# Kernel tuning notes

Hardware: AMD Instinct MI355X
Metric: run time of the kernel (lower is better)

## Reference

```python
import jax, jax.numpy as jnp
import numpy as np

EPS = 1e-06

def _feature_map(x):
    # elu(x) + 1, positive feature map
    return jax.nn.elu(x) + 1.0

def setup_inputs() -> dict:
    key = jax.random.key(0)
    k1, k2, k3 = jax.random.split(key, 3)
    B, L, d_k, d_v = 2, 4096, 128, 128
    Q = jax.random.normal(k1, (B, L, d_k), dtype=jnp.float32)
    K = jax.random.normal(k2, (B, L, d_k), dtype=jnp.float32)
    V = jax.random.normal(k3, (B, L, d_v), dtype=jnp.float32)
    return {"Q": Q, "K": K, "V": V}

def reference(Q, K, V):
    # Causal linear attention (ELU feature map).
    # out_l = phi(Q_l) @ sum_{j<=l} phi(K_j)^T V_j
    # Z_l   = phi(Q_l) . sum_{j<=l} phi(K_j)
    phiQ = _feature_map(Q)                       # (B, L, dk)
    phiK = _feature_map(K)                       # (B, L, dk)
    # cumulative KV state: (B, L, dk, dv) -- parallel replacement of the
    # original per-step bmm loop
    KV = jnp.cumsum(phiK[..., :, None] * V[..., None, :], axis=1)
    out = jnp.einsum('blk,blkv->blv', phiQ, KV)  # (B, L, dv)
    Kc = jnp.cumsum(phiK, axis=1)                # (B, L, dk)
    Z = jnp.einsum('blk,blk->bl', phiQ, Kc)[..., None]  # (B, L, 1)
    return out / (Z + EPS)
```

## Files before the change

### kernel.cpp

```cpp
#include <hip/hip_runtime.h>


#define EPS 1e-6f

constexpr int Bc = 2;
constexpr int L  = 4096;
constexpr int D  = 128;
constexpr int C  = 128;
constexpr int NC = L / C;
constexpr int P  = 136;

typedef short sh8 __attribute__((ext_vector_type(8)));
typedef float f4  __attribute__((ext_vector_type(4)));

__device__ __forceinline__ float phi(float x) {
    return x > 0.0f ? x + 1.0f : __expf(x);
}
__device__ __forceinline__ unsigned short f2bf(float f) {
    unsigned u = __float_as_uint(f);
    return (unsigned short)((u + 0x7FFFu + ((u >> 16) & 1u)) >> 16);
}
__device__ __forceinline__ float bf2f(unsigned short h) {
    return __uint_as_float(((unsigned)h) << 16);
}
__device__ __forceinline__ sh8 splat1() {
    sh8 s;
#pragma unroll
    for (int j = 0; j < 8; ++j) s[j] = (short)0x3F80;
    return s;
}

__global__ __launch_bounds__(512) void k_prep(
    const float* __restrict__ Q, const float* __restrict__ K,
    const float* __restrict__ V,
    unsigned short* __restrict__ QB, unsigned short* __restrict__ KB,
    unsigned short* __restrict__ KT, unsigned short* __restrict__ VT) {
    const int c = blockIdx.x, b = blockIdx.y, zz = blockIdx.z;
    const int tid = threadIdx.x;
    __shared__ __align__(16) unsigned short sT[128 * P];
    const size_t base  = ((size_t)b * L + (size_t)c * C) * D;
    const size_t tbase = ((size_t)(b * NC + c)) * D * D;

    if (zz == 0) {
        for (int k = 0; k < 8; ++k) {
            int fi = tid + 512 * k;
            int l = fi >> 5, i4 = fi & 31;
            float4 d = *(const float4*)(K + base + (size_t)l * D + i4 * 4);
            unsigned short e0 = f2bf(phi(d.x)), e1 = f2bf(phi(d.y));
            unsigned short e2 = f2bf(phi(d.z)), e3 = f2bf(phi(d.w));
            uint2 pk;
            pk.x = (unsigned)e0 | ((unsigned)e1 << 16);
            pk.y = (unsigned)e2 | ((unsigned)e3 << 16);
            *(uint2*)(KB + base + (size_t)l * D + i4 * 4) = pk;
            int blk = (((l >> 3) + i4) & 15) * 8 + (l & 7);
            sT[(i4 * 4 + 0) * P + blk] = e0;
            sT[(i4 * 4 + 1) * P + blk] = e1;
            sT[(i4 * 4 + 2) * P + blk] = e2;
            sT[(i4 * 4 + 3) * P + blk] = e3;
        }
        __syncthreads();
        for (int k = 0; k < 4; ++k) {
            int fi = tid + 512 * k;
            int i = fi >> 4, lch = fi & 15;
            uint4 dd = *(const uint4*)(sT + i * P + (((lch + (i >> 2)) & 15) * 8));
            *(uint4*)(KT + tbase + (size_t)i * D + lch * 8) = dd;
        }
    } else {
        for (int k = 0; k < 8; ++k) {
            int fi = tid + 512 * k;
            int l = fi >> 5, i4 = fi & 31;
            float4 d = *(const float4*)(V + base + (size_t)l * D + i4 * 4);
            int blk = (((l >> 3) + i4) & 15) * 8 + (l & 7);
            sT[(i4 * 4 + 0) * P + blk] = f2bf(d.x);
            sT[(i4 * 4 + 1) * P + blk] = f2bf(d.y);
            sT[(i4 * 4 + 2) * P + blk] = f2bf(d.z);
            sT[(i4 * 4 + 3) * P + blk] = f2bf(d.w);
        }
        for (int k = 0; k < 8; ++k) {
            int fi = tid + 512 * k;
            int l = fi >> 5, i4 = fi & 31;
            float4 d = *(const float4*)(Q + base + (size_t)l * D + i4 * 4);
            uint2 pk;
            pk.x = (unsigned)f2bf(phi(d.x)) | ((unsigned)f2bf(phi(d.y)) << 16);
            pk.y = (unsigned)f2bf(phi(d.z)) | ((unsigned)f2bf(phi(d.w)) << 16);
            *(uint2*)(QB + base + (size_t)l * D + i4 * 4) = pk;
        }
        __syncthreads();
        for (int k = 0; k < 4; ++k) {
            int fi = tid + 512 * k;
            int v = fi >> 4, lch = fi & 15;
            uint4 dd = *(const uint4*)(sT + v * P + (((lch + (v >> 2)) & 15) * 8));
            *(uint4*)(VT + tbase + (size_t)v * D + lch * 8) = dd;
        }
    }
}

__global__ __launch_bounds__(512) void k1(
    const unsigned short* __restrict__ KT, const unsigned short* __restrict__ VT,
    unsigned short* __restrict__ SB, float* __restrict__ Ksum) {
    const int c = blockIdx.x, b = blockIdx.y, vs = blockIdx.z;
    const int tid = threadIdx.x;
    __shared__ __align__(16) unsigned short sA[64 * P];
    __shared__ __align__(16) unsigned short sKb[128 * P];
    const size_t tbase = ((size_t)(b * NC + c)) * D * D;

    const uint4* vtg = (const uint4*)(VT + tbase + (size_t)vs * 64 * D);
    for (int k = 0; k < 2; ++k) {
        int fi = tid + 512 * k;
        int v = fi >> 4, ch = fi & 15;
        *(uint4*)(sA + v * P + ch * 8) = vtg[fi];
    }
    const uint4* ktg = (const uint4*)(KT + tbase);
    for (int k = 0; k < 4; ++k) {
        int fi = tid + 512 * k;
        int i = fi >> 4, ch = fi & 15;
        *(uint4*)(sKb + i * P + ch * 8) = ktg[fi];
    }
    __syncthreads();

    const int w = tid >> 6, lane = tid & 63;
    const int r = lane & 15, q = lane >> 4;
    const int rbase = (w & 3) * 16;
    const int cbase = (w >> 2) * 64;
    const bool doZ = (vs == 0) && ((w & 3) == 0);
    const sh8 az = splat1();

    f4 acc[4], kz[4];
#pragma unroll
    for (int f = 0; f < 4; ++f) { acc[f] = {0.f,0.f,0.f,0.f}; kz[f] = {0.f,0.f,0.f,0.f}; }
#pragma unroll
    for (int ks = 0; ks < 4; ++ks) {
        sh8 a = *(const sh8*)(sA + (rbase + r) * P + ks * 32 + q * 8);
#pragma unroll
        for (int f = 0; f < 4; ++f) {
            sh8 bb = *(const sh8*)(sKb + (cbase + f * 16 + r) * P + ks * 32 + q * 8);
            acc[f] = __builtin_amdgcn_mfma_f32_16x16x32_bf16(a, bb, acc[f], 0, 0, 0);
            if (doZ) kz[f] = __builtin_amdgcn_mfma_f32_16x16x32_bf16(az, bb, kz[f], 0, 0, 0);
        }
    }
    unsigned short* out = SB + tbase;
#pragma unroll
    for (int f = 0; f < 4; ++f) {
        int i = cbase + f * 16 + r;
#pragma unroll
        for (int e = 0; e < 4; ++e) {
            int v = vs * 64 + rbase + q * 4 + e;
            out[(size_t)v * D + i] = f2bf(acc[f][e]);
        }
    }
    if (doZ && q == 0) {
#pragma unroll
        for (int f = 0; f < 4; ++f)
            Ksum[((size_t)(b * NC + c)) * D + cbase + f * 16 + r] = kz[f][0];
    }
}

__global__ __launch_bounds__(256) void k_scan(unsigned short* __restrict__ SB,
                                              float* __restrict__ Ksum) {
    const int SD = D * D;
    int idx = blockIdx.x * 256 + threadIdx.x;
    if (idx < Bc * SD) {
        int b = idx / SD, e = idx % SD;
        size_t off0 = (size_t)b * NC * SD + e;
        unsigned short vals[NC];
#pragma unroll
        for (int c = 0; c < NC; ++c) vals[c] = SB[off0 + (size_t)c * SD];
        float run = 0.0f;
#pragma unroll
        for (int c = 0; c < NC; ++c) {
            SB[off0 + (size_t)c * SD] = f2bf(run);
            run += bf2f(vals[c]);
        }
    } else if (idx < Bc * SD + Bc * D) {
        int rr = idx - Bc * SD;
        int b = rr >> 7, i = rr & 127;
        size_t off0 = (size_t)b * NC * D + i;
        float vals[NC];
#pragma unroll
        for (int c = 0; c < NC; ++c) vals[c] = Ksum[off0 + (size_t)c * D];
        float run = 0.0f;
#pragma unroll
        for (int c = 0; c < NC; ++c) {
            Ksum[off0 + (size_t)c * D] = run;
            run += vals[c];
        }
    }
}

__global__ __launch_bounds__(512) void k_out(
    const unsigned short* __restrict__ QB, const unsigned short* __restrict__ KB,
    const unsigned short* __restrict__ VT, const unsigned short* __restrict__ SB,
    const float* __restrict__ Ksum, float* __restrict__ Out) {
    const int c = blockIdx.x, b = blockIdx.y, rs = blockIdx.z;
    const int tid = threadIdx.x;
    __shared__ __align__(16) unsigned short sQ[32 * P];
    __shared__ __align__(16) unsigned short sKb[128 * P];
    __shared__ __align__(16) unsigned short sV[128 * P];
    __shared__ __align__(16) unsigned short sAm[32 * P];
    __shared__ float sZ[32];
    const size_t base  = ((size_t)b * L + (size_t)c * C) * D;
    const size_t tbase = ((size_t)(b * NC + c)) * D * D;
    const size_t kb    = ((size_t)(b * NC + c)) * D;

    {
        const uint4* qg = (const uint4*)(QB + base + (size_t)rs * 32 * D);
        int fi = tid;
        *(uint4*)(sQ + (fi >> 4) * P + (fi & 15) * 8) = qg[fi];
        const uint4* kg = (const uint4*)(KB + base);
        for (int k = 0; k < 4; ++k) {
            int f2 = tid + 512 * k;
            *(uint4*)(sKb + (f2 >> 4) * P + (f2 & 15) * 8) = kg[f2];
        }
        const uint4* vg = (const uint4*)(VT + tbase);
        for (int k = 0; k < 4; ++k) {
            int f2 = tid + 512 * k;
            *(uint4*)(sV + (f2 >> 4) * P + (f2 & 15) * 8) = vg[f2];
        }
    }
    __syncthreads();

    const int w = tid >> 6, lane = tid & 63;
    const int r = lane & 15, q = lane >> 4;
    const int rbase = (w & 1) * 16;
    const int cq = w >> 1, cbase = cq * 32;
    const bool doZ = (cq == 3);

    sh8 bzk[4];
    if (doZ) {
#pragma unroll
        for (int ks = 0; ks < 4; ++ks) {
            float4 f0 = *(const float4*)(Ksum + kb + ks * 32 + q * 8);
            float4 f1 = *(const float4*)(Ksum + kb + ks * 32 + q * 8 + 4);
            sh8 t;
            t[0] = (short)f2bf(f0.x); t[1] = (short)f2bf(f0.y);
            t[2] = (short)f2bf(f0.z); t[3] = (short)f2bf(f0.w);
            t[4] = (short)f2bf(f1.x); t[5] = (short)f2bf(f1.y);
            t[6] = (short)f2bf(f1.z); t[7] = (short)f2bf(f1.w);
            bzk[ks] = t;
        }
    }

    f4 a2[2];
#pragma unroll
    for (int f = 0; f < 2; ++f) a2[f] = {0.f,0.f,0.f,0.f};
#pragma unroll
    for (int ks = 0; ks < 4; ++ks) {
        sh8 a = *(const sh8*)(sQ + (rbase + r) * P + ks * 32 + q * 8);
#pragma unroll
        for (int f = 0; f < 2; ++f) {
            sh8 bb = *(const sh8*)(sKb + (cbase + f * 16 + r) * P + ks * 32 + q * 8);
            a2[f] = __builtin_amdgcn_mfma_f32_16x16x32_bf16(a, bb, a2[f], 0, 0, 0);
        }
    }
#pragma unroll
    for (int f = 0; f < 2; ++f) {
        int j = cbase + f * 16 + r;
#pragma unroll
        for (int e = 0; e < 4; ++e) {
            int lr = rbase + q * 4 + e;
            sAm[lr * P + j] = f2bf((j <= rs * 32 + lr) ? a2[f][e] : 0.0f);
        }
    }
    __syncthreads();

    {
        const uint4* sg = (const uint4*)(SB + tbase);
        for (int k = 0; k < 4; ++k) {
            int f2 = tid + 512 * k;
            *(uint4*)(sKb + (f2 >> 4) * P + (f2 & 15) * 8) = sg[f2];
        }
    }

    f4 acc[2], zacc = {0.f,0.f,0.f,0.f};
#pragma unroll
    for (int f = 0; f < 2; ++f) acc[f] = {0.f,0.f,0.f,0.f};
    const sh8 bones = splat1();
#pragma unroll
    for (int ks = 0; ks < 4; ++ks) {
        sh8 a = *(const sh8*)(sAm + (rbase + r) * P + ks * 32 + q * 8);
#pragma unroll
        for (int f = 0; f < 2; ++f) {
            sh8 bb = *(const sh8*)(sV + (cbase + f * 16 + r) * P + ks * 32 + q * 8);
            acc[f] = __builtin_amdgcn_mfma_f32_16x16x32_bf16(a, bb, acc[f], 0, 0, 0);
        }
        if (doZ) zacc = __builtin_amdgcn_mfma_f32_16x16x32_bf16(a, bones, zacc, 0, 0, 0);
    }
    __syncthreads();

#pragma unroll
    for (int ks = 0; ks < 4; ++ks) {
        sh8 a = *(const sh8*)(sQ + (rbase + r) * P + ks * 32 + q * 8);
#pragma unroll
        for (int f = 0; f < 2; ++f) {
            sh8 bb = *(const sh8*)(sKb + (cbase + f * 16 + r) * P + ks * 32 + q * 8);
            acc[f] = __builtin_amdgcn_mfma_f32_16x16x32_bf16(a, bb, acc[f], 0, 0, 0);
        }
        if (doZ) zacc = __builtin_amdgcn_mfma_f32_16x16x32_bf16(a, bzk[ks], zacc, 0, 0, 0);
    }
    if (doZ && r == 0) {
#pragma unroll
        for (int e = 0; e < 4; ++e) sZ[rbase + q * 4 + e] = zacc[e] + EPS;
    }
    __syncthreads();

#pragma unroll
    for (int f = 0; f < 2; ++f) {
        int v = cbase + f * 16 + r;
#pragma unroll
        for (int e = 0; e < 4; ++e) {
            int lr = rbase + q * 4 + e;
            Out[base + (size_t)(rs * 32 + lr) * D + v] = acc[f][e] / sZ[lr];
        }
    }
}

extern "C" void kernel_launch(void* const* d_in, const int* in_sizes, int n_in,
                              void* d_out, int out_size, void* d_ws, size_t ws_size,
                              hipStream_t stream) {
    const float* Q = (const float*)d_in[0];
    const float* K = (const float*)d_in[1];
    const float* V = (const float*)d_in[2];
    float* Out = (float*)d_out;
    constexpr size_t NE = (size_t)Bc * L * D;
    char* w = (char*)d_ws;
    unsigned short* SBw  = (unsigned short*)(w);
    float*          Ksum = (float*)(w + NE * 2);
    unsigned short* QB   = (unsigned short*)(w + NE * 2 + (size_t)Bc * NC * D * 4);
    unsigned short* KB   = QB + NE;
    unsigned short* KT   = KB + NE;
    unsigned short* VT   = KT + NE;

    k_prep<<<dim3(NC, Bc, 2), 512, 0, stream>>>(Q, K, V, QB, KB, KT, VT);
    k1<<<dim3(NC, Bc, 2), 512, 0, stream>>>(KT, VT, SBw, Ksum);
    int total = Bc * D * D + Bc * D;
    k_scan<<<dim3((total + 255) / 256), 256, 0, stream>>>(SBw, Ksum);
    k_out<<<dim3(NC, Bc, 4), 512, 0, stream>>>(QB, KB, VT, SBw, Ksum, Out);
}
```

Baseline: 82.20 us.

## Fuse bf16 conversion and feature map into consumer kernels, drop prep kernel

Removes the separate preprocessing kernel that wrote bf16 copies and transposes of phi(Q), phi(K) and V to workspace. The chunk-state kernel and the output kernel now read fp32 inputs directly, apply the feature map, convert to bf16, and transpose into swizzled shared memory themselves, with MFMA operand reads adjusted to the swizzle. This saves one launch and the intermediate global write/read traffic. In exchange, K and V are read and converted redundantly across the z-split blocks (up to four times for K and V in the output kernel) and fp32 loads double the bytes per element.

Result: faster. 77.74 us (-5.4%).

```diff
diff --git a/kernel.cpp b/kernel.cpp
--- a/kernel.cpp
+++ b/kernel.cpp
@@ -23,6 +23,9 @@
 __device__ __forceinline__ float bf2f(unsigned short h) {
     return __uint_as_float(((unsigned)h) << 16);
 }
+__device__ __forceinline__ unsigned packbf(float a, float b) {
+    return (unsigned)f2bf(a) | ((unsigned)f2bf(b) << 16);
+}
 __device__ __forceinline__ sh8 splat1() {
     sh8 s;
 #pragma unroll
@@ -30,91 +33,34 @@
     return s;
 }
 
-__global__ __launch_bounds__(512) void k_prep(
-    const float* __restrict__ Q, const float* __restrict__ K,
-    const float* __restrict__ V,
-    unsigned short* __restrict__ QB, unsigned short* __restrict__ KB,
-    unsigned short* __restrict__ KT, unsigned short* __restrict__ VT) {
-    const int c = blockIdx.x, b = blockIdx.y, zz = blockIdx.z;
-    const int tid = threadIdx.x;
-    __shared__ __align__(16) unsigned short sT[128 * P];
-    const size_t base  = ((size_t)b * L + (size_t)c * C) * D;
-    const size_t tbase = ((size_t)(b * NC + c)) * D * D;
-
-    if (zz == 0) {
-        for (int k = 0; k < 8; ++k) {
-            int fi = tid + 512 * k;
-            int l = fi >> 5, i4 = fi & 31;
-            float4 d = *(const float4*)(K + base + (size_t)l * D + i4 * 4);
-            unsigned short e0 = f2bf(phi(d.x)), e1 = f2bf(phi(d.y));
-            unsigned short e2 = f2bf(phi(d.z)), e3 = f2bf(phi(d.w));
-            uint2 pk;
-            pk.x = (unsigned)e0 | ((unsigned)e1 << 16);
-            pk.y = (unsigned)e2 | ((unsigned)e3 << 16);
-            *(uint2*)(KB + base + (size_t)l * D + i4 * 4) = pk;
-            int blk = (((l >> 3) + i4) & 15) * 8 + (l & 7);
-            sT[(i4 * 4 + 0) * P + blk] = e0;
-            sT[(i4 * 4 + 1) * P + blk] = e1;
-            sT[(i4 * 4 + 2) * P + blk] = e2;
-            sT[(i4 * 4 + 3) * P + blk] = e3;
-        }
-        __syncthreads();
-        for (int k = 0; k < 4; ++k) {
-            int fi = tid + 512 * k;
-            int i = fi >> 4, lch = fi & 15;
-            uint4 dd = *(const uint4*)(sT + i * P + (((lch + (i >> 2)) & 15) * 8));
-            *(uint4*)(KT + tbase + (size_t)i * D + lch * 8) = dd;
-        }
-    } else {
-        for (int k = 0; k < 8; ++k) {
-            int fi = tid + 512 * k;
-            int l = fi >> 5, i4 = fi & 31;
-            float4 d = *(const float4*)(V + base + (size_t)l * D + i4 * 4);
-            int blk = (((l >> 3) + i4) & 15) * 8 + (l & 7);
-            sT[(i4 * 4 + 0) * P + blk] = f2bf(d.x);
-            sT[(i4 * 4 + 1) * P + blk] = f2bf(d.y);
-            sT[(i4 * 4 + 2) * P + blk] = f2bf(d.z);
-            sT[(i4 * 4 + 3) * P + blk] = f2bf(d.w);
-        }
-        for (int k = 0; k < 8; ++k) {
-            int fi = tid + 512 * k;
-            int l = fi >> 5, i4 = fi & 31;
-            float4 d = *(const float4*)(Q + base + (size_t)l * D + i4 * 4);
-            uint2 pk;
-            pk.x = (unsigned)f2bf(phi(d.x)) | ((unsigned)f2bf(phi(d.y)) << 16);
-            pk.y = (unsigned)f2bf(phi(d.z)) | ((unsigned)f2bf(phi(d.w)) << 16);
-            *(uint2*)(QB + base + (size_t)l * D + i4 * 4) = pk;
-        }
-        __syncthreads();
-        for (int k = 0; k < 4; ++k) {
-            int fi = tid + 512 * k;
-            int v = fi >> 4, lch = fi & 15;
-            uint4 dd = *(const uint4*)(sT + v * P + (((lch + (v >> 2)) & 15) * 8));
-            *(uint4*)(VT + tbase + (size_t)v * D + lch * 8) = dd;
-        }
-    }
-}
-
 __global__ __launch_bounds__(512) void k1(
-    const unsigned short* __restrict__ KT, const unsigned short* __restrict__ VT,
+    const float* __restrict__ K, const float* __restrict__ V,
     unsigned short* __restrict__ SB, float* __restrict__ Ksum) {
     const int c = blockIdx.x, b = blockIdx.y, vs = blockIdx.z;
     const int tid = threadIdx.x;
-    __shared__ __align__(16) unsigned short sA[64 * P];
-    __shared__ __align__(16) unsigned short sKb[128 * P];
-    const size_t tbase = ((size_t)(b * NC + c)) * D * D;
-
-    const uint4* vtg = (const uint4*)(VT + tbase + (size_t)vs * 64 * D);
-    for (int k = 0; k < 2; ++k) {
-        int fi = tid + 512 * k;
-        int v = fi >> 4, ch = fi & 15;
-        *(uint4*)(sA + v * P + ch * 8) = vtg[fi];
-    }
-    const uint4* ktg = (const uint4*)(KT + tbase);
+    __shared__ __align__(16) unsigned short sVT[64 * P];
+    __shared__ __align__(16) unsigned short sKT[128 * P];
+    const size_t base = ((size_t)b * L + (size_t)c * C) * D;
+
     for (int k = 0; k < 4; ++k) {
         int fi = tid + 512 * k;
-        int i = fi >> 4, ch = fi & 15;
-        *(uint4*)(sKb + i * P + ch * 8) = ktg[fi];
+        int l = fi >> 4, c4 = fi & 15;
+        float4 vd = *(const float4*)(V + base + (size_t)l * D + vs * 64 + c4 * 4);
+        int blk = (((l >> 3) + c4) & 15) * 8 + (l & 7);
+        sVT[(c4 * 4 + 0) * P + blk] = f2bf(vd.x);
+        sVT[(c4 * 4 + 1) * P + blk] = f2bf(vd.y);
+        sVT[(c4 * 4 + 2) * P + blk] = f2bf(vd.z);
+        sVT[(c4 * 4 + 3) * P + blk] = f2bf(vd.w);
+    }
+    for (int k = 0; k < 8; ++k) {
+        int fi = tid + 512 * k;
+        int l = fi >> 5, i4 = fi & 31;
+        float4 kd = *(const float4*)(K + base + (size_t)l * D + i4 * 4);
+        int blk = (((l >> 3) + i4) & 15) * 8 + (l & 7);
+        sKT[(i4 * 4 + 0) * P + blk] = f2bf(phi(kd.x));
+        sKT[(i4 * 4 + 1) * P + blk] = f2bf(phi(kd.y));
+        sKT[(i4 * 4 + 2) * P + blk] = f2bf(phi(kd.z));
+        sKT[(i4 * 4 + 3) * P + blk] = f2bf(phi(kd.w));
     }
     __syncthreads();
 
@@ -122,23 +68,26 @@
     const int r = lane & 15, q = lane >> 4;
     const int rbase = (w & 3) * 16;
     const int cbase = (w >> 2) * 64;
-    const bool doZ = (vs == 0) && ((w & 3) == 0);
-    const sh8 az = splat1();
+    const bool doK = ((w & 3) == 0);
+    const sh8 ones = splat1();
 
     f4 acc[4], kz[4];
 #pragma unroll
     for (int f = 0; f < 4; ++f) { acc[f] = {0.f,0.f,0.f,0.f}; kz[f] = {0.f,0.f,0.f,0.f}; }
 #pragma unroll
     for (int ks = 0; ks < 4; ++ks) {
-        sh8 a = *(const sh8*)(sA + (rbase + r) * P + ks * 32 + q * 8);
+        int kq = ks * 4 + q;
+        int vr = rbase + r;
+        sh8 a = *(const sh8*)(sVT + vr * P + ((kq + (vr >> 2)) & 15) * 8);
 #pragma unroll
         for (int f = 0; f < 4; ++f) {
-            sh8 bb = *(const sh8*)(sKb + (cbase + f * 16 + r) * P + ks * 32 + q * 8);
-            acc[f] = __builtin_amdgcn_mfma_f32_16x16x32_bf16(a, bb, acc[f], 0, 0, 0);
-            if (doZ) kz[f] = __builtin_amdgcn_mfma_f32_16x16x32_bf16(az, bb, kz[f], 0, 0, 0);
-        }
-    }
-    unsigned short* out = SB + tbase;
+            int ir = cbase + f * 16 + r;
+            sh8 bk = *(const sh8*)(sKT + ir * P + ((kq + (ir >> 2)) & 15) * 8);
+            acc[f] = __builtin_amdgcn_mfma_f32_16x16x32_bf16(a, bk, acc[f], 0, 0, 0);
+            if (doK) kz[f] = __builtin_amdgcn_mfma_f32_16x16x32_bf16(ones, bk, kz[f], 0, 0, 0);
+        }
+    }
+    unsigned short* out = SB + ((size_t)(b * NC + c)) * D * D;
 #pragma unroll
     for (int f = 0; f < 4; ++f) {
         int i = cbase + f * 16 + r;
@@ -148,7 +97,7 @@
             out[(size_t)v * D + i] = f2bf(acc[f][e]);
         }
     }
-    if (doZ && q == 0) {
+    if (doK && q == 0 && vs == 0) {
 #pragma unroll
         for (int f = 0; f < 4; ++f)
             Ksum[((size_t)(b * NC + c)) * D + cbase + f * 16 + r] = kz[f][0];
@@ -188,34 +137,43 @@
 }
 
 __global__ __launch_bounds__(512) void k_out(
-    const unsigned short* __restrict__ QB, const unsigned short* __restrict__ KB,
-    const unsigned short* __restrict__ VT, const unsigned short* __restrict__ SB,
+    const float* __restrict__ Q, const float* __restrict__ K,
+    const float* __restrict__ V, const unsigned short* __restrict__ SB,
     const float* __restrict__ Ksum, float* __restrict__ Out) {
     const int c = blockIdx.x, b = blockIdx.y, rs = blockIdx.z;
     const int tid = threadIdx.x;
     __shared__ __align__(16) unsigned short sQ[32 * P];
-    __shared__ __align__(16) unsigned short sKb[128 * P];
-    __shared__ __align__(16) unsigned short sV[128 * P];
+    __shared__ __align__(16) unsigned short sK[128 * P];
+    __shared__ __align__(16) unsigned short sVT[128 * P];
     __shared__ __align__(16) unsigned short sAm[32 * P];
     __shared__ float sZ[32];
     const size_t base  = ((size_t)b * L + (size_t)c * C) * D;
-    const size_t tbase = ((size_t)(b * NC + c)) * D * D;
+    const size_t tbase = ((size_t)(b * NC + c)) * (size_t)D * D;
     const size_t kb    = ((size_t)(b * NC + c)) * D;
 
-    {
-        const uint4* qg = (const uint4*)(QB + base + (size_t)rs * 32 * D);
-        int fi = tid;
-        *(uint4*)(sQ + (fi >> 4) * P + (fi & 15) * 8) = qg[fi];
-        const uint4* kg = (const uint4*)(KB + base);
-        for (int k = 0; k < 4; ++k) {
-            int f2 = tid + 512 * k;
-            *(uint4*)(sKb + (f2 >> 4) * P + (f2 & 15) * 8) = kg[f2];
-        }
-        const uint4* vg = (const uint4*)(VT + tbase);
-        for (int k = 0; k < 4; ++k) {
-            int f2 = tid + 512 * k;
-            *(uint4*)(sV + (f2 >> 4) * P + (f2 & 15) * 8) = vg[f2];
-        }
+    for (int k = 0; k < 2; ++k) {
+        int fi = tid + 512 * k;
+        int row = fi >> 5, c4 = fi & 31;
+        float4 qd = *(const float4*)(Q + base + (size_t)(rs * 32 + row) * D + c4 * 4);
+        uint2 pq; pq.x = packbf(phi(qd.x), phi(qd.y)); pq.y = packbf(phi(qd.z), phi(qd.w));
+        *(uint2*)(sQ + row * P + c4 * 4) = pq;
+    }
+    for (int k = 0; k < 8; ++k) {
+        int fi = tid + 512 * k;
+        int row = fi >> 5, c4 = fi & 31;
+        float4 kd = *(const float4*)(K + base + (size_t)row * D + c4 * 4);
+        uint2 pk; pk.x = packbf(phi(kd.x), phi(kd.y)); pk.y = packbf(phi(kd.z), phi(kd.w));
+        *(uint2*)(sK + row * P + c4 * 4) = pk;
+    }
+    for (int k = 0; k < 8; ++k) {
+        int fi = tid + 512 * k;
+        int l = fi >> 5, i4 = fi & 31;
+        float4 vd = *(const float4*)(V + base + (size_t)l * D + i4 * 4);
+        int blk = (((l >> 3) + i4) & 15) * 8 + (l & 7);
+        sVT[(i4 * 4 + 0) * P + blk] = f2bf(vd.x);
+        sVT[(i4 * 4 + 1) * P + blk] = f2bf(vd.y);
+        sVT[(i4 * 4 + 2) * P + blk] = f2bf(vd.z);
+        sVT[(i4 * 4 + 3) * P + blk] = f2bf(vd.w);
     }
     __syncthreads();
 
@@ -248,7 +206,7 @@
         sh8 a = *(const sh8*)(sQ + (rbase + r) * P + ks * 32 + q * 8);
 #pragma unroll
         for (int f = 0; f < 2; ++f) {
-            sh8 bb = *(const sh8*)(sKb + (cbase + f * 16 + r) * P + ks * 32 + q * 8);
+            sh8 bb = *(const sh8*)(sK + (cbase + f * 16 + r) * P + ks * 32 + q * 8);
             a2[f] = __builtin_amdgcn_mfma_f32_16x16x32_bf16(a, bb, a2[f], 0, 0, 0);
         }
     }
@@ -258,7 +216,7 @@
 #pragma unroll
         for (int e = 0; e < 4; ++e) {
             int lr = rbase + q * 4 + e;
-            sAm[lr * P + j] = f2bf((j <= rs * 32 + lr) ? a2[f][e] : 0.0f);
+            sAm[lr * P + j] = f2bf((j <= rs * 32 + lr) ? a2[f][e] : 0.f);
         }
     }
     __syncthreads();
@@ -267,23 +225,25 @@
         const uint4* sg = (const uint4*)(SB + tbase);
         for (int k = 0; k < 4; ++k) {
             int f2 = tid + 512 * k;
-            *(uint4*)(sKb + (f2 >> 4) * P + (f2 & 15) * 8) = sg[f2];
+            *(uint4*)(sK + (f2 >> 4) * P + (f2 & 15) * 8) = sg[f2];
         }
     }
 
     f4 acc[2], zacc = {0.f,0.f,0.f,0.f};
 #pragma unroll
     for (int f = 0; f < 2; ++f) acc[f] = {0.f,0.f,0.f,0.f};
-    const sh8 bones = splat1();
-#pragma unroll
-    for (int ks = 0; ks < 4; ++ks) {
+    const sh8 ones = splat1();
+#pragma unroll
+    for (int ks = 0; ks < 4; ++ks) {
+        int kq = ks * 4 + q;
         sh8 a = *(const sh8*)(sAm + (rbase + r) * P + ks * 32 + q * 8);
 #pragma unroll
         for (int f = 0; f < 2; ++f) {
-            sh8 bb = *(const sh8*)(sV + (cbase + f * 16 + r) * P + ks * 32 + q * 8);
-            acc[f] = __builtin_amdgcn_mfma_f32_16x16x32_bf16(a, bb, acc[f], 0, 0, 0);
-        }
-        if (doZ) zacc = __builtin_amdgcn_mfma_f32_16x16x32_bf16(a, bones, zacc, 0, 0, 0);
+            int vr = cbase + f * 16 + r;
+            sh8 bv = *(const sh8*)(sVT + vr * P + ((kq + (vr >> 2)) & 15) * 8);
+            acc[f] = __builtin_amdgcn_mfma_f32_16x16x32_bf16(a, bv, acc[f], 0, 0, 0);
+        }
+        if (doZ) zacc = __builtin_amdgcn_mfma_f32_16x16x32_bf16(a, ones, zacc, 0, 0, 0);
     }
     __syncthreads();
 
@@ -292,8 +252,8 @@
         sh8 a = *(const sh8*)(sQ + (rbase + r) * P + ks * 32 + q * 8);
 #pragma unroll
         for (int f = 0; f < 2; ++f) {
-            sh8 bb = *(const sh8*)(sKb + (cbase + f * 16 + r) * P + ks * 32 + q * 8);
-            acc[f] = __builtin_amdgcn_mfma_f32_16x16x32_bf16(a, bb, acc[f], 0, 0, 0);
+            sh8 bs = *(const sh8*)(sK + (cbase + f * 16 + r) * P + ks * 32 + q * 8);
+            acc[f] = __builtin_amdgcn_mfma_f32_16x16x32_bf16(a, bs, acc[f], 0, 0, 0);
         }
         if (doZ) zacc = __builtin_amdgcn_mfma_f32_16x16x32_bf16(a, bzk[ks], zacc, 0, 0, 0);
     }
@@ -321,18 +281,11 @@
     const float* K = (const float*)d_in[1];
     const float* V = (const float*)d_in[2];
     float* Out = (float*)d_out;
-    constexpr size_t NE = (size_t)Bc * L * D;
-    char* w = (char*)d_ws;
-    unsigned short* SBw  = (unsigned short*)(w);
-    float*          Ksum = (float*)(w + NE * 2);
-    unsigned short* QB   = (unsigned short*)(w + NE * 2 + (size_t)Bc * NC * D * 4);
-    unsigned short* KB   = QB + NE;
-    unsigned short* KT   = KB + NE;
-    unsigned short* VT   = KT + NE;
-
-    k_prep<<<dim3(NC, Bc, 2), 512, 0, stream>>>(Q, K, V, QB, KB, KT, VT);
-    k1<<<dim3(NC, Bc, 2), 512, 0, stream>>>(KT, VT, SBw, Ksum);
+    unsigned short* SBw = (unsigned short*)d_ws;
+    float* Ksum = (float*)((char*)d_ws + (size_t)Bc * NC * D * D * 2);
+
+    k1<<<dim3(NC, Bc, 2), 512, 0, stream>>>(K, V, SBw, Ksum);
     int total = Bc * D * D + Bc * D;
     k_scan<<<dim3((total + 255) / 256), 256, 0, stream>>>(SBw, Ksum);
-    k_out<<<dim3(NC, Bc, 4), 512, 0, stream>>>(QB, KB, VT, SBw, Ksum, Out);
-}
+    k_out<<<dim3(NC, Bc, 4), 512, 0, stream>>>(Q, K, V, SBw, Ksum, Out);
+}
```
